# Kernel tuning notes

Hardware: AMD Instinct MI355X
Metric: run time of the kernel (lower is better)

Reference implementation:

```python
import jax, jax.numpy as jnp
import numpy as np

EPS = 1e-5

def conv1d(x, w, b, pad):
    # x: (B,Cin,T), w: (Cout,Cin,K)
    y = jax.lax.conv_general_dilated(x, w, (1,), [(pad, pad)],
                                     dimension_numbers=('NCW', 'OIW', 'NCW'))
    return y + b[None, :, None]

def group_norm(x, scale, bias, groups):
    B, C, T = x.shape
    xg = x.reshape(B, groups, C // groups, T)
    mu = xg.mean(axis=(2, 3), keepdims=True)
    var = xg.var(axis=(2, 3), keepdims=True)
    xn = ((xg - mu) * jax.lax.rsqrt(var + EPS)).reshape(B, C, T)
    return xn * scale[None, :, None] + bias[None, :, None]

def setup_inputs() -> dict:
    key = jax.random.key(0)
    ks = jax.random.split(key, 16)
    T, B = 1024, 128
    class_size, style_size, char_style_size = 80, 256, 64
    hidden, n_out = 128, 1
    cin = class_size + style_size + char_style_size  # 400
    def w(k, shape, fan_in):
        return jax.random.normal(k, shape, jnp.float32) * (1.0 / np.sqrt(fan_in))
    inp = {
        'input': jax.random.normal(ks[0], (T, B, class_size), jnp.float32),
        'g_style': jax.random.normal(ks[1], (B, style_size), jnp.float32),
        'spacing_style': jax.random.normal(ks[2], (B, 8), jnp.float32),
        'char_style': jax.random.normal(ks[3], (B, class_size, char_style_size), jnp.float32),
        'conv1_w': w(ks[4], (hidden, cin, 3), cin * 3),
        'conv1_b': jnp.zeros((hidden,), jnp.float32),
        'gn1_s': jnp.ones((hidden,), jnp.float32),
        'gn1_b': jnp.zeros((hidden,), jnp.float32),
        'conv2_w': w(ks[5], (hidden // 2, hidden, 3), hidden * 3),
        'conv2_b': jnp.zeros((hidden // 2,), jnp.float32),
        'gn2_s': jnp.ones((hidden // 2,), jnp.float32),
        'gn2_b': jnp.zeros((hidden // 2,), jnp.float32),
        'conv3_w': w(ks[6], (hidden // 4, hidden // 2, 3), (hidden // 2) * 3),
        'conv3_b': jnp.zeros((hidden // 4,), jnp.float32),
        'gn3_s': jnp.ones((hidden // 4,), jnp.float32),
        'gn3_b': jnp.zeros((hidden // 4,), jnp.float32),
        'conv4_w': w(ks[7], (n_out, hidden // 4, 1), hidden // 4),
        'conv4_b': jnp.zeros((n_out,), jnp.float32),
        'mean': jnp.full((1, n_out), 2.0, jnp.float32),
        'std': jnp.full((1, n_out), 1.0, jnp.float32),
    }
    return inp

def reference(input, g_style, spacing_style, char_style,
              conv1_w, conv1_b, gn1_s, gn1_b,
              conv2_w, conv2_b, gn2_s, gn2_b,
              conv3_w, conv3_b, gn3_s, gn3_b,
              conv4_w, conv4_b, mean, std):
    T, B, _ = input.shape
    # vectorized char-style gather (replaces the python double loop)
    text_chars = jnp.argmax(input, axis=2)                      # (T,B)
    input_style = char_style[jnp.arange(B)[None, :], text_chars]  # (T,B,Dc)
    gs = jnp.broadcast_to(g_style[None], (T,) + g_style.shape)    # (T,B,Ds)
    x = jnp.concatenate([input, gs, input_style], axis=2)         # (T,B,Cin)
    x = x.transpose(1, 2, 0)                                      # (B,Cin,T)
    x = jax.nn.relu(group_norm(conv1d(x, conv1_w, conv1_b, 1), gn1_s, gn1_b, 32))
    x = jax.nn.relu(group_norm(conv1d(x, conv2_w, conv2_b, 1), gn2_s, gn2_b, 32))
    x = jax.nn.relu(group_norm(conv1d(x, conv3_w, conv3_b, 1), gn3_s, gn3_b, 32))
    x = conv1d(x, conv4_w, conv4_b, 0)                            # (B,n_out,T)
    out = x.transpose(2, 0, 1)                                    # (T,B,n_out)
    return out * std + mean
```

## Files before the change

### kernel.cpp

```cpp
#include <hip/hip_runtime.h>
#include <hip/hip_bf16.h>

#define T_LEN 1024
#define BATCH 128
#define NM 131072

typedef __attribute__((ext_vector_type(8))) short short8;
typedef __attribute__((ext_vector_type(4))) float f32x4;

__device__ __forceinline__ float b2f(ushort u) {
  union { uint i; float f; } c; c.i = ((uint)u) << 16; return c.f;
}
__device__ __forceinline__ ushort f2b(float f) {
  __hip_bfloat16 h = __float2bfloat16(f);
  return *reinterpret_cast<ushort*>(&h);
}
__device__ __forceinline__ uint pack2(float a, float b) {
  return (uint)f2b(a) | ((uint)f2b(b) << 16);
}

__global__ __launch_bounds__(256) void k_prep(const float* __restrict__ gsty,
    const float* __restrict__ w1, const float* __restrict__ b1,
    const float* __restrict__ w2, const float* __restrict__ w3,
    float* __restrict__ Gfull, float* __restrict__ Gk0, float* __restrict__ Gk2,
    ushort* __restrict__ Wp1, ushort* __restrict__ Wp2, ushort* __restrict__ Wp3) {
  int bid = blockIdx.x, tid = threadIdx.x;
  if (bid < 128) {
    int b = bid;
    __shared__ float gl[256];
    gl[tid] = gsty[b*256 + tid];
    __syncthreads();
    if (tid < 128) {
      int o = tid;
      const float* wr = w1 + (size_t)o*1200 + 240;
      float s0 = 0.f, s1 = 0.f, s2 = 0.f;
      for (int c = 0; c < 256; ++c) {
        float g = gl[c];
        s0 += wr[c*3+0]*g; s1 += wr[c*3+1]*g; s2 += wr[c*3+2]*g;
      }
      Gk0[b*128+o] = s0;
      Gk2[b*128+o] = s2;
      Gfull[b*128+o] = s0 + s1 + s2 + b1[o];
    }
  } else {
    int e = (bid - 128)*256 + tid;
    if (e < 61440) {
      int o = e / 480, r = e % 480, k = r / 160, c = r % 160;
      float v = 0.f;
      if (c < 80)       v = w1[(size_t)o*1200 + c*3 + k];
      else if (c >= 96) v = w1[(size_t)o*1200 + (336 + (c-96))*3 + k];
      Wp1[e] = f2b(v);
    } else if (e < 61440 + 24576) {
      int e2 = e - 61440;
      int o = e2/384, r = e2%384, k = r/128, c = r%128;
      Wp2[e2] = f2b(w2[(size_t)o*384 + c*3 + k]);
    } else if (e < 61440 + 24576 + 6144) {
      int e3 = e - 61440 - 24576;
      int o = e3/192, r = e3%192, k = r/64, c = r%64;
      Wp3[e3] = f2b(w3[(size_t)o*192 + c*3 + k]);
    }
  }
}

__device__ __forceinline__ void c1_ldg(const float* __restrict__ inp, const float* __restrict__ cs,
                                       const int* idxs, int b, int cc, int t0, int task,
                                       float4& fa, float4& fb) {
  int r = task >> 2, q = task & 3;
  int t = t0 - 1 + r;
  fa = make_float4(0.f,0.f,0.f,0.f); fb = fa;
  if (t >= 0 && t < T_LEN) {
    const float* src;
    if (cc < 3) {
      int c8 = cc*32 + q*8;
      if (c8 >= 80) return;
      src = inp + ((size_t)t*BATCH + b)*80 + c8;
    } else {
      int jc = idxs[r];
      src = cs + ((size_t)b*80 + jc)*64 + (cc-3)*32 + q*8;
    }
    fa = *(const float4*)src;
    fb = *(const float4*)(src + 4);
  }
}
__device__ __forceinline__ void amax8(float& best, int& bi, float4 fa, float4 fb, int base, bool valid) {
  if (!valid) return;
  float v[8] = {fa.x, fa.y, fa.z, fa.w, fb.x, fb.y, fb.z, fb.w};
  #pragma unroll
  for (int i = 0; i < 8; ++i)
    if (v[i] > best) { best = v[i]; bi = base + i; }
}
__device__ __forceinline__ uint4 packf(float4 a, float4 b) {
  uint4 p;
  p.x = pack2(a.x, a.y); p.y = pack2(a.z, a.w);
  p.z = pack2(b.x, b.y); p.w = pack2(b.z, b.w);
  return p;
}
__device__ __forceinline__ short8 c1_ldw(const ushort* Wp1, int cc, int task) {
  int o = task / 12, seg = task % 12;
  int k = seg >> 2, oct = seg & 3;
  return *(const short8*)(Wp1 + (size_t)o*480 + k*160 + cc*32 + oct*8);
}
__device__ __forceinline__ void c1_wrx(ushort (*Xsb)[40], int task, uint4 v) {
  int r = task >> 2, q = task & 3;
  *(uint4*)&Xsb[r][q*8] = v;
}
__device__ __forceinline__ void c1_wrw(ushort (*Wsb)[104], int task, short8 v) {
  int o = task / 12, seg = task % 12;
  *(short8*)&Wsb[o][seg*8] = v;
}

__global__ __launch_bounds__(256) void k_conv1(const float* __restrict__ inp, const float* __restrict__ cs,
    const ushort* __restrict__ Wp1,
    const float* __restrict__ Gfull, const float* __restrict__ Gk0, const float* __restrict__ Gk2,
    ushort* __restrict__ y1, float2* __restrict__ part1) {
  __shared__ __align__(16) ushort Xs[2][130][40];
  __shared__ __align__(16) ushort Ws[2][128][104];
  __shared__ float gf[128], g0v[128], g2v[128];
  __shared__ float ps[4][128], pq[4][128];
  __shared__ int idxs[130];
  int b = blockIdx.x, tt = blockIdx.y;
  int t0 = tt * 128;
  int tid = threadIdx.x, lane = tid & 63, wave = tid >> 6;
  int ln = lane & 15, lq = lane >> 4, wt = wave * 32;
  int q = tid & 3, u = tid >> 2;

  if (tid < 128) {
    gf[tid]  = Gfull[b*128 + tid];
    g0v[tid] = Gk0[b*128 + tid];
    g2v[tid] = Gk2[b*128 + tid];
  }
  f32x4 acc[2][8];
  #pragma unroll
  for (int m = 0; m < 2; ++m)
    #pragma unroll
    for (int n = 0; n < 8; ++n) { f32x4 z = {0.f,0.f,0.f,0.f}; acc[m][n] = z; }

  float4 fa0, fb0, fa1, fb1, fa2, fb2;
  short8 rw[6];
  float bm0 = -1e30f, bm1 = -1e30f, bm2 = -1e30f;
  int ib0 = 0, ib1 = 0, ib2 = 0;

  c1_ldg(inp, cs, idxs, b, 0, t0, tid, fa0, fb0);
  c1_ldg(inp, cs, idxs, b, 0, t0, tid + 256, fa1, fb1);
  if (tid < 8) c1_ldg(inp, cs, idxs, b, 0, t0, tid + 512, fa2, fb2);
  amax8(bm0, ib0, fa0, fb0, q*8, true);
  amax8(bm1, ib1, fa1, fb1, q*8, true);
  if (tid < 8) amax8(bm2, ib2, fa2, fb2, q*8, true);
  #pragma unroll
  for (int i = 0; i < 6; ++i) rw[i] = c1_ldw(Wp1, 0, tid + i*256);
  c1_wrx(Xs[0], tid, packf(fa0, fb0));
  c1_wrx(Xs[0], tid + 256, packf(fa1, fb1));
  if (tid < 8) c1_wrx(Xs[0], tid + 512, packf(fa2, fb2));
  #pragma unroll
  for (int i = 0; i < 6; ++i) c1_wrw(Ws[0], tid + i*256, rw[i]);
  __syncthreads();

  for (int cc = 0; cc < 5; ++cc) {
    bool more = (cc < 4);
    if (more) {
      c1_ldg(inp, cs, idxs, b, cc+1, t0, tid, fa0, fb0);
      c1_ldg(inp, cs, idxs, b, cc+1, t0, tid + 256, fa1, fb1);
      if (tid < 8) c1_ldg(inp, cs, idxs, b, cc+1, t0, tid + 512, fa2, fb2);
      if (cc < 2) {
        int base = (cc+1)*32 + q*8;
        bool valid = (cc+1 < 2) || (q < 2);
        amax8(bm0, ib0, fa0, fb0, base, valid);
        amax8(bm1, ib1, fa1, fb1, base, valid);
        if (tid < 8) amax8(bm2, ib2, fa2, fb2, base, valid);
      }
      if (cc == 1) {
        #pragma unroll
        for (int d = 1; d <= 2; d <<= 1) {
          float ob; int oi;
          ob = __shfl_xor(bm0, d); oi = __shfl_xor(ib0, d);
          if (ob > bm0 || (ob == bm0 && oi < ib0)) { bm0 = ob; ib0 = oi; }
          ob = __shfl_xor(bm1, d); oi = __shfl_xor(ib1, d);
          if (ob > bm1 || (ob == bm1 && oi < ib1)) { bm1 = ob; ib1 = oi; }
          ob = __shfl_xor(bm2, d); oi = __shfl_xor(ib2, d);
          if (ob > bm2 || (ob == bm2 && oi < ib2)) { bm2 = ob; ib2 = oi; }
        }
        if (q == 0) { idxs[u] = ib0; idxs[u + 64] = ib1; }
        if (tid < 8 && (tid & 3) == 0) idxs[128 + (tid >> 2)] = ib2;
      }
      #pragma unroll
      for (int i = 0; i < 6; ++i) rw[i] = c1_ldw(Wp1, cc+1, tid + i*256);
    }
    int cur = cc & 1;
    #pragma unroll
    for (int k = 0; k < 3; ++k) {
      short8 a0 = *(const short8*)&Xs[cur][wt + ln + k][lq*8];
      short8 a1 = *(const short8*)&Xs[cur][wt + 16 + ln + k][lq*8];
      #pragma unroll
      for (int nt = 0; nt < 8; ++nt) {
        short8 bb = *(const short8*)&Ws[cur][nt*16 + ln][k*32 + lq*8];
        acc[0][nt] = __builtin_amdgcn_mfma_f32_16x16x32_bf16(a0, bb, acc[0][nt], 0, 0, 0);
        acc[1][nt] = __builtin_amdgcn_mfma_f32_16x16x32_bf16(a1, bb, acc[1][nt], 0, 0, 0);
      }
    }
    if (more) {
      int nxt = cur ^ 1;
      c1_wrx(Xs[nxt], tid, packf(fa0, fb0));
      c1_wrx(Xs[nxt], tid + 256, packf(fa1, fb1));
      if (tid < 8) c1_wrx(Xs[nxt], tid + 512, packf(fa2, fb2));
      #pragma unroll
      for (int i = 0; i < 6; ++i) c1_wrw(Ws[nxt], tid + i*256, rw[i]);
    }
    __syncthreads();
  }

  #pragma unroll
  for (int nt = 0; nt < 8; ++nt) {
    int o = nt*16 + ln;
    float add = gf[o];
    float s = 0.f, sq = 0.f;
    #pragma unroll
    for (int mt = 0; mt < 2; ++mt) {
      int tb = t0 + wt + mt*16 + lq*4;
      float vv[4];
      #pragma unroll
      for (int r = 0; r < 4; ++r) {
        float v = acc[mt][nt][r] + add;
        int t = tb + r;
        if (t == 0) v -= g0v[o];
        if (t == T_LEN-1) v -= g2v[o];
        vv[r] = v; s += v; sq += v*v;
      }
      uint2 pk;
      pk.x = pack2(vv[0], vv[1]);
      pk.y = pack2(vv[2], vv[3]);
      *(uint2*)(y1 + ((size_t)b*128 + o)*T_LEN + tb) = pk;
    }
    s  += __shfl_xor(s, 16);  s  += __shfl_xor(s, 32);
    sq += __shfl_xor(sq, 16); sq += __shfl_xor(sq, 32);
    if (lane < 16) { ps[wave][o] = s; pq[wave][o] = sq; }
  }
  __syncthreads();
  if (tid < 128) {
    float S = ps[0][tid]+ps[1][tid]+ps[2][tid]+ps[3][tid];
    float Q = pq[0][tid]+pq[1][tid]+pq[2][tid]+pq[3][tid];
    part1[((size_t)b*128 + tid)*8 + tt] = make_float2(S, Q);
  }
}

__device__ __forceinline__ short8 mid_ldw(const ushort* Wp, int cin, int cc, int task) {
  int o = task / 12, seg = task % 12;
  int k = seg >> 2, oct = seg & 3;
  return *(const short8*)(Wp + ((size_t)o*3 + k)*cin + cc*32 + oct*8);
}
__device__ __forceinline__ void mid_wrw(ushort (*Wsb)[104], int task, short8 v) {
  int o = task / 12, seg = task % 12;
  *(short8*)&Wsb[o][seg*8] = v;
}

template<int NC, int CO, int NT, int CPG>
__global__ __launch_bounds__(256) void k_convmid(const ushort* __restrict__ xin,
    const ushort* __restrict__ Wp, const float* __restrict__ bias,
    const float2* __restrict__ partin, const float* __restrict__ gs, const float* __restrict__ gb,
    ushort* __restrict__ yout, float2* __restrict__ part) {
  constexpr int CIN = NC*32;
  constexpr int NG = CIN/CPG;
  __shared__ __align__(16) ushort Xs[2][130][40];
  __shared__ __align__(16) ushort Ws[2][CO][104];
  __shared__ float2 affl[CIN];
  __shared__ float ssb[CIN], qqb[CIN];
  __shared__ float2 gmr[NG];
  __shared__ float bl[CO];
  __shared__ float ps[4][CO], pq[4][CO];
  int b = blockIdx.x, tt = blockIdx.y, t0 = tt*128;
  int tid = threadIdx.x, lane = tid & 63, wave = tid >> 6;
  int ln = lane & 15, lq = lane >> 4, wt = wave*32;
  int cp = (tid & 15)*2, j = tid >> 4;
  int er = (tid < 32) ? 0 : 129, eci = tid & 31;
  const ushort* xb = xin + (size_t)b * CIN * T_LEN;

  if (tid < CIN) {
    const float2* p = partin + (size_t)(b*CIN + tid)*8;
    float S = 0.f, Q = 0.f;
    #pragma unroll
    for (int j2 = 0; j2 < 8; ++j2) { float2 v = p[j2]; S += v.x; Q += v.y; }
    ssb[tid] = S; qqb[tid] = Q;
  }
  if (tid < CO)  bl[tid]  = bias[tid];

  f32x4 acc[2][NT];
  #pragma unroll
  for (int m = 0; m < 2; ++m)
    #pragma unroll
    for (int n = 0; n < NT; ++n) { f32x4 z = {0.f,0.f,0.f,0.f}; acc[m][n] = z; }

  short8 v0, v1;
  ushort ev = 0;
  short8 rw0, rw1, rw2;
  int te = t0 - 1 + er;

  {
    const ushort* s0 = xb + (size_t)cp * T_LEN + t0 + j*8;
    v0 = *(const short8*)s0;
    v1 = *(const short8*)(s0 + T_LEN);
    ev = 0;
    if (tid < 64 && te >= 0 && te < T_LEN) ev = xb[(size_t)eci * T_LEN + te];
    rw0 = mid_ldw(Wp, CIN, 0, tid);
    if constexpr (CO == 64) {
      rw1 = mid_ldw(Wp, CIN, 0, tid + 256);
      rw2 = mid_ldw(Wp, CIN, 0, tid + 512);
    } else {
      if (tid < 128) rw1 = mid_ldw(Wp, CIN, 0, tid + 256);
    }
  }
  __syncthreads();
  if (tid < NG) {
    float S = 0.f, Q = 0.f;
    #pragma unroll
    for (int ci = 0; ci < CPG; ++ci) { S += ssb[tid*CPG+ci]; Q += qqb[tid*CPG+ci]; }
    float invn = 1.f / (float)(CPG * T_LEN);
    float m = S * invn;
    float var = Q * invn - m*m;
    gmr[tid] = make_float2(m, rsqrtf(var + 1e-5f));
  }
  __syncthreads();
  if (tid < CIN) {
    float2 mr = gmr[tid / CPG];
    float a = mr.y * gs[tid];
    affl[tid] = make_float2(a, gb[tid] - mr.x * a);
  }
  __syncthreads();
  {
    float2 A0 = affl[cp], A1 = affl[cp+1];
    #pragma unroll
    for (int e = 0; e < 8; ++e) {
      float f0 = fmaxf(0.f, b2f((ushort)v0[e])*A0.x + A0.y);
      float f1 = fmaxf(0.f, b2f((ushort)v1[e])*A1.x + A1.y);
      *(uint*)&Xs[0][1 + j*8 + e][cp] = pack2(f0, f1);
    }
    if (tid < 64) {
      ushort val = 0;
      if (te >= 0 && te < T_LEN) { float2 A = affl[eci]; val = f2b(fmaxf(0.f, b2f(ev)*A.x + A.y)); }
      Xs[0][er][eci] = val;
    }
    mid_wrw(Ws[0], tid, rw0);
    if constexpr (CO == 64) {
      mid_wrw(Ws[0], tid + 256, rw1);
      mid_wrw(Ws[0], tid + 512, rw2);
    } else {
      if (tid < 128) mid_wrw(Ws[0], tid + 256, rw1);
    }
  }
  __syncthreads();

  for (int cc = 0; cc < NC; ++cc) {
    bool more = (cc + 1 < NC);
    if (more) {
      const ushort* s0 = xb + (size_t)((cc+1)*32 + cp) * T_LEN + t0 + j*8;
      v0 = *(const short8*)s0;
      v1 = *(const short8*)(s0 + T_LEN);
      ev = 0;
      if (tid < 64 && te >= 0 && te < T_LEN) ev = xb[(size_t)((cc+1)*32 + eci) * T_LEN + te];
      rw0 = mid_ldw(Wp, CIN, cc+1, tid);
      if constexpr (CO == 64) {
        rw1 = mid_ldw(Wp, CIN, cc+1, tid + 256);
        rw2 = mid_ldw(Wp, CIN, cc+1, tid + 512);
      } else {
        if (tid < 128) rw1 = mid_ldw(Wp, CIN, cc+1, tid + 256);
      }
    }
    int cur = cc & 1;
    #pragma unroll
    for (int k = 0; k < 3; ++k) {
      short8 a0 = *(const short8*)&Xs[cur][wt + ln + k][lq*8];
      short8 a1 = *(const short8*)&Xs[cur][wt + 16 + ln + k][lq*8];
      #pragma unroll
      for (int nt = 0; nt < NT; ++nt) {
        short8 bb = *(const short8*)&Ws[cur][nt*16 + ln][k*32 + lq*8];
        acc[0][nt] = __builtin_amdgcn_mfma_f32_16x16x32_bf16(a0, bb, acc[0][nt], 0, 0, 0);
        acc[1][nt] = __builtin_amdgcn_mfma_f32_16x16x32_bf16(a1, bb, acc[1][nt], 0, 0, 0);
      }
    }
    if (more) {
      int nxt = cur ^ 1;
      float2 A0 = affl[(cc+1)*32 + cp], A1 = affl[(cc+1)*32 + cp + 1];
      #pragma unroll
      for (int e = 0; e < 8; ++e) {
        float f0 = fmaxf(0.f, b2f((ushort)v0[e])*A0.x + A0.y);
        float f1 = fmaxf(0.f, b2f((ushort)v1[e])*A1.x + A1.y);
        *(uint*)&Xs[nxt][1 + j*8 + e][cp] = pack2(f0, f1);
      }
      if (tid < 64) {
        ushort val = 0;
        if (te >= 0 && te < T_LEN) { float2 A = affl[(cc+1)*32 + eci]; val = f2b(fmaxf(0.f, b2f(ev)*A.x + A.y)); }
        Xs[nxt][er][eci] = val;
      }
      mid_wrw(Ws[nxt], tid, rw0);
      if constexpr (CO == 64) {
        mid_wrw(Ws[nxt], tid + 256, rw1);
        mid_wrw(Ws[nxt], tid + 512, rw2);
      } else {
        if (tid < 128) mid_wrw(Ws[nxt], tid + 256, rw1);
      }
    }
    __syncthreads();
  }

  #pragma unroll
  for (int nt = 0; nt < NT; ++nt) {
    int o = nt*16 + ln;
    float add = bl[o];
    float s = 0.f, sq = 0.f;
    #pragma unroll
    for (int mt = 0; mt < 2; ++mt) {
      int tb = t0 + wt + mt*16 + lq*4;
      float vv[4];
      #pragma unroll
      for (int r = 0; r < 4; ++r) {
        float v = acc[mt][nt][r] + add;
        vv[r] = v; s += v; sq += v*v;
      }
      uint2 pk;
      pk.x = pack2(vv[0], vv[1]);
      pk.y = pack2(vv[2], vv[3]);
      *(uint2*)(yout + ((size_t)b*CO + o)*T_LEN + tb) = pk;
    }
    s  += __shfl_xor(s, 16);  s  += __shfl_xor(s, 32);
    sq += __shfl_xor(sq, 16); sq += __shfl_xor(sq, 32);
    if (lane < 16) { ps[wave][o] = s; pq[wave][o] = sq; }
  }
  __syncthreads();
  if (tid < CO) {
    float S = ps[0][tid]+ps[1][tid]+ps[2][tid]+ps[3][tid];
    float Q = pq[0][tid]+pq[1][tid]+pq[2][tid]+pq[3][tid];
    part[((size_t)b*CO + tid)*8 + tt] = make_float2(S, Q);
  }
}

__global__ __launch_bounds__(256) void k_final(const ushort* __restrict__ y3, const float2* __restrict__ part3,
    const float* __restrict__ s3, const float* __restrict__ b3,
    const float* __restrict__ w4, const float* __restrict__ b4,
    const float* __restrict__ mn, const float* __restrict__ sd, float* __restrict__ out) {
  int b = blockIdx.x;
  int t = blockIdx.y * 256 + threadIdx.x;
  __shared__ float wl[32];
  __shared__ float2 al[32];
  if (threadIdx.x < 32) {
    int c = threadIdx.x;
    const float2* p = part3 + (size_t)(b*32 + c)*8;
    float S = 0.f, Q = 0.f;
    #pragma unroll
    for (int j = 0; j < 8; ++j) { float2 v = p[j]; S += v.x; Q += v.y; }
    float invn = 1.f / (float)T_LEN;
    float m = S * invn;
    float var = Q * invn - m*m;
    float rs = rsqrtf(var + 1e-5f);
    float a = rs * s3[c];
    al[c] = make_float2(a, b3[c] - m*a);
    wl[c] = w4[c];
  }
  __syncthreads();
  float s = b4[0];
  #pragma unroll 8
  for (int c = 0; c < 32; ++c) {
    float v = b2f(y3[((size_t)b*32 + c)*T_LEN + t]);
    float2 A = al[c];
    s += wl[c] * fmaxf(0.f, v*A.x + A.y);
  }
  out[(size_t)t*BATCH + b] = s*sd[0] + mn[0];
}

extern "C" void kernel_launch(void* const* d_in, const int* in_sizes, int n_in,
                              void* d_out, int out_size, void* d_ws, size_t ws_size,
                              hipStream_t stream) {
  const float* inp  = (const float*)d_in[0];
  const float* gsty = (const float*)d_in[1];
  const float* cs   = (const float*)d_in[3];
  const float* w1   = (const float*)d_in[4];
  const float* b1   = (const float*)d_in[5];
  const float* gn1s = (const float*)d_in[6];
  const float* gn1b = (const float*)d_in[7];
  const float* w2   = (const float*)d_in[8];
  const float* b2   = (const float*)d_in[9];
  const float* gn2s = (const float*)d_in[10];
  const float* gn2b = (const float*)d_in[11];
  const float* w3   = (const float*)d_in[12];
  const float* b3   = (const float*)d_in[13];
  const float* gn3s = (const float*)d_in[14];
  const float* gn3b = (const float*)d_in[15];
  const float* w4   = (const float*)d_in[16];
  const float* b4   = (const float*)d_in[17];
  const float* mn   = (const float*)d_in[18];
  const float* sd   = (const float*)d_in[19];
  float* out = (float*)d_out;
  ushort* wsu = (ushort*)d_ws;

  ushort* Wp1 = wsu;
  ushort* Wp2 = Wp1 + 61440;
  ushort* Wp3 = Wp2 + 24576;
  float* Gfull = (float*)(Wp3 + 6144);
  float* Gk0   = Gfull + 16384;
  float* Gk2   = Gk0 + 16384;
  ushort* y1 = (ushort*)(Gk2 + 16384);
  ushort* y2 = y1 + (size_t)NM*128;
  ushort* y3 = y2 + (size_t)NM*64;
  float2* part1 = (float2*)(y3 + (size_t)NM*32);
  float2* part2 = part1 + 131072;
  float2* part3 = part2 + 65536;

  k_prep<<<488, 256, 0, stream>>>(gsty, w1, b1, w2, w3,
                                  Gfull, Gk0, Gk2, Wp1, Wp2, Wp3);
  k_conv1<<<dim3(128,8), 256, 0, stream>>>(inp, cs, Wp1, Gfull, Gk0, Gk2, y1, part1);
  k_convmid<4,64,4,4><<<dim3(128,8), 256, 0, stream>>>(y1, Wp2, b2, part1, gn1s, gn1b, y2, part2);
  k_convmid<2,32,2,2><<<dim3(128,8), 256, 0, stream>>>(y2, Wp3, b3, part2, gn2s, gn2b, y3, part3);
  k_final<<<dim3(128,4), 256, 0, stream>>>(y3, part3, gn3s, gn3b, w4, b4, mn, sd, out);
}
```

Baseline: 89.51 us.

## Store intermediate activations time-major via LDS-staged transposed epilogue

The bf16 intermediate activations between conv layers change from channel-major (B,C,T) to time-major (B,T,C). The epilogues stage outputs in shared memory (reusing the weight buffer) and write 16-byte coalesced rows. The mid-conv loader then reads contiguous 32-channel slices per time step, which replaces the strided per-channel loads and the separate halo scalar loads, and the final kernel reads each time row with four vector loads. The cost is an extra LDS round trip and barrier in the epilogue, and possible bank conflicts from the scattered 2-byte LDS stores.

```diff
diff --git a/kernel.cpp b/kernel.cpp
--- a/kernel.cpp
+++ b/kernel.cpp
@@ -208,6 +208,8 @@
     __syncthreads();
   }
 
+  ushort* Ts = &Ws[0][0][0];
+  constexpr int TP = 136;
   #pragma unroll
   for (int nt = 0; nt < 8; ++nt) {
     int o = nt*16 + ln;
@@ -215,26 +217,29 @@
     float s = 0.f, sq = 0.f;
     #pragma unroll
     for (int mt = 0; mt < 2; ++mt) {
-      int tb = t0 + wt + mt*16 + lq*4;
-      float vv[4];
+      int tl = wt + mt*16 + lq*4;
       #pragma unroll
       for (int r = 0; r < 4; ++r) {
         float v = acc[mt][nt][r] + add;
-        int t = tb + r;
+        int t = t0 + tl + r;
         if (t == 0) v -= g0v[o];
         if (t == T_LEN-1) v -= g2v[o];
-        vv[r] = v; s += v; sq += v*v;
-      }
-      uint2 pk;
-      pk.x = pack2(vv[0], vv[1]);
-      pk.y = pack2(vv[2], vv[3]);
-      *(uint2*)(y1 + ((size_t)b*128 + o)*T_LEN + tb) = pk;
+        s += v; sq += v*v;
+        Ts[(tl + r)*TP + o] = f2b(v);
+      }
     }
     s  += __shfl_xor(s, 16);  s  += __shfl_xor(s, 32);
     sq += __shfl_xor(sq, 16); sq += __shfl_xor(sq, 32);
     if (lane < 16) { ps[wave][o] = s; pq[wave][o] = sq; }
   }
   __syncthreads();
+  ushort* yb = y1 + ((size_t)b*1024 + t0)*128;
+  #pragma unroll
+  for (int it = 0; it < 8; ++it) {
+    int i = it*256 + tid;
+    int tl = i >> 4, c8 = (i & 15) * 8;
+    *(uint4*)(yb + tl*128 + c8) = *(const uint4*)(&Ts[tl*TP + c8]);
+  }
   if (tid < 128) {
     float S = ps[0][tid]+ps[1][tid]+ps[2][tid]+ps[3][tid];
     float Q = pq[0][tid]+pq[1][tid]+pq[2][tid]+pq[3][tid];
@@ -242,6 +247,32 @@
   }
 }
 
+__device__ __forceinline__ uint4 mid_ldx(const ushort* __restrict__ xb, int CINv, int cc, int t0, int task) {
+  int r = task >> 2, q = task & 3;
+  int t = t0 - 1 + r;
+  if (t >= 0 && t < T_LEN) return *(const uint4*)(xb + (size_t)t*CINv + cc*32 + q*8);
+  return make_uint4(0u,0u,0u,0u);
+}
+__device__ __forceinline__ void mid_wrx(ushort (*Xsb)[40], const float2* affl, int cbase,
+                                        int t0, int task, uint4 v) {
+  int r = task >> 2, q = task & 3;
+  int t = t0 - 1 + r;
+  uint4 w = make_uint4(0u,0u,0u,0u);
+  if (t >= 0 && t < T_LEN) {
+    const ushort* sv = (const ushort*)&v;
+    uint o[4];
+    #pragma unroll
+    for (int e = 0; e < 4; ++e) {
+      float2 A0 = affl[cbase + q*8 + 2*e];
+      float2 A1 = affl[cbase + q*8 + 2*e + 1];
+      float f0 = fmaxf(0.f, b2f(sv[2*e])*A0.x + A0.y);
+      float f1 = fmaxf(0.f, b2f(sv[2*e+1])*A1.x + A1.y);
+      o[e] = pack2(f0, f1);
+    }
+    w = make_uint4(o[0], o[1], o[2], o[3]);
+  }
+  *(uint4*)&Xsb[r][q*8] = w;
+}
 __device__ __forceinline__ short8 mid_ldw(const ushort* Wp, int cin, int cc, int task) {
   int o = task / 12, seg = task % 12;
   int k = seg >> 2, oct = seg & 3;
@@ -259,6 +290,7 @@
     ushort* __restrict__ yout, float2* __restrict__ part) {
   constexpr int CIN = NC*32;
   constexpr int NG = CIN/CPG;
+  constexpr int TP = CO + 8;
   __shared__ __align__(16) ushort Xs[2][130][40];
   __shared__ __align__(16) ushort Ws[2][CO][104];
   __shared__ float2 affl[CIN];
@@ -269,9 +301,7 @@
   int b = blockIdx.x, tt = blockIdx.y, t0 = tt*128;
   int tid = threadIdx.x, lane = tid & 63, wave = tid >> 6;
   int ln = lane & 15, lq = lane >> 4, wt = wave*32;
-  int cp = (tid & 15)*2, j = tid >> 4;
-  int er = (tid < 32) ? 0 : 129, eci = tid & 31;
-  const ushort* xb = xin + (size_t)b * CIN * T_LEN;
+  const ushort* xb = xin + (size_t)b * 1024 * CIN;
 
   if (tid < CIN) {
     const float2* p = partin + (size_t)(b*CIN + tid)*8;
@@ -288,24 +318,18 @@
     #pragma unroll
     for (int n = 0; n < NT; ++n) { f32x4 z = {0.f,0.f,0.f,0.f}; acc[m][n] = z; }
 
-  short8 v0, v1;
-  ushort ev = 0;
+  uint4 rx0, rx1, rx2;
   short8 rw0, rw1, rw2;
-  int te = t0 - 1 + er;
-
-  {
-    const ushort* s0 = xb + (size_t)cp * T_LEN + t0 + j*8;
-    v0 = *(const short8*)s0;
-    v1 = *(const short8*)(s0 + T_LEN);
-    ev = 0;
-    if (tid < 64 && te >= 0 && te < T_LEN) ev = xb[(size_t)eci * T_LEN + te];
-    rw0 = mid_ldw(Wp, CIN, 0, tid);
-    if constexpr (CO == 64) {
-      rw1 = mid_ldw(Wp, CIN, 0, tid + 256);
-      rw2 = mid_ldw(Wp, CIN, 0, tid + 512);
-    } else {
-      if (tid < 128) rw1 = mid_ldw(Wp, CIN, 0, tid + 256);
-    }
+
+  rx0 = mid_ldx(xb, CIN, 0, t0, tid);
+  rx1 = mid_ldx(xb, CIN, 0, t0, tid + 256);
+  if (tid < 8) rx2 = mid_ldx(xb, CIN, 0, t0, tid + 512);
+  rw0 = mid_ldw(Wp, CIN, 0, tid);
+  if constexpr (CO == 64) {
+    rw1 = mid_ldw(Wp, CIN, 0, tid + 256);
+    rw2 = mid_ldw(Wp, CIN, 0, tid + 512);
+  } else {
+    if (tid < 128) rw1 = mid_ldw(Wp, CIN, 0, tid + 256);
   }
   __syncthreads();
   if (tid < NG) {
@@ -324,37 +348,24 @@
     affl[tid] = make_float2(a, gb[tid] - mr.x * a);
   }
   __syncthreads();
-  {
-    float2 A0 = affl[cp], A1 = affl[cp+1];
-    #pragma unroll
-    for (int e = 0; e < 8; ++e) {
-      float f0 = fmaxf(0.f, b2f((ushort)v0[e])*A0.x + A0.y);
-      float f1 = fmaxf(0.f, b2f((ushort)v1[e])*A1.x + A1.y);
-      *(uint*)&Xs[0][1 + j*8 + e][cp] = pack2(f0, f1);
-    }
-    if (tid < 64) {
-      ushort val = 0;
-      if (te >= 0 && te < T_LEN) { float2 A = affl[eci]; val = f2b(fmaxf(0.f, b2f(ev)*A.x + A.y)); }
-      Xs[0][er][eci] = val;
-    }
-    mid_wrw(Ws[0], tid, rw0);
-    if constexpr (CO == 64) {
-      mid_wrw(Ws[0], tid + 256, rw1);
-      mid_wrw(Ws[0], tid + 512, rw2);
-    } else {
-      if (tid < 128) mid_wrw(Ws[0], tid + 256, rw1);
-    }
+  mid_wrx(Xs[0], affl, 0, t0, tid, rx0);
+  mid_wrx(Xs[0], affl, 0, t0, tid + 256, rx1);
+  if (tid < 8) mid_wrx(Xs[0], affl, 0, t0, tid + 512, rx2);
+  mid_wrw(Ws[0], tid, rw0);
+  if constexpr (CO == 64) {
+    mid_wrw(Ws[0], tid + 256, rw1);
+    mid_wrw(Ws[0], tid + 512, rw2);
+  } else {
+    if (tid < 128) mid_wrw(Ws[0], tid + 256, rw1);
   }
   __syncthreads();
 
   for (int cc = 0; cc < NC; ++cc) {
     bool more = (cc + 1 < NC);
     if (more) {
-      const ushort* s0 = xb + (size_t)((cc+1)*32 + cp) * T_LEN + t0 + j*8;
-      v0 = *(const short8*)s0;
-      v1 = *(const short8*)(s0 + T_LEN);
-      ev = 0;
-      if (tid < 64 && te >= 0 && te < T_LEN) ev = xb[(size_t)((cc+1)*32 + eci) * T_LEN + te];
+      rx0 = mid_ldx(xb, CIN, cc+1, t0, tid);
+      rx1 = mid_ldx(xb, CIN, cc+1, t0, tid + 256);
+      if (tid < 8) rx2 = mid_ldx(xb, CIN, cc+1, t0, tid + 512);
       rw0 = mid_ldw(Wp, CIN, cc+1, tid);
       if constexpr (CO == 64) {
         rw1 = mid_ldw(Wp, CIN, cc+1, tid + 256);
@@ -377,18 +388,9 @@
     }
     if (more) {
       int nxt = cur ^ 1;
-      float2 A0 = affl[(cc+1)*32 + cp], A1 = affl[(cc+1)*32 + cp + 1];
-      #pragma unroll
-      for (int e = 0; e < 8; ++e) {
-        float f0 = fmaxf(0.f, b2f((ushort)v0[e])*A0.x + A0.y);
-        float f1 = fmaxf(0.f, b2f((ushort)v1[e])*A1.x + A1.y);
-        *(uint*)&Xs[nxt][1 + j*8 + e][cp] = pack2(f0, f1);
-      }
-      if (tid < 64) {
-        ushort val = 0;
-        if (te >= 0 && te < T_LEN) { float2 A = affl[(cc+1)*32 + eci]; val = f2b(fmaxf(0.f, b2f(ev)*A.x + A.y)); }
-        Xs[nxt][er][eci] = val;
-      }
+      mid_wrx(Xs[nxt], affl, (cc+1)*32, t0, tid, rx0);
+      mid_wrx(Xs[nxt], affl, (cc+1)*32, t0, tid + 256, rx1);
+      if (tid < 8) mid_wrx(Xs[nxt], affl, (cc+1)*32, t0, tid + 512, rx2);
       mid_wrw(Ws[nxt], tid, rw0);
       if constexpr (CO == 64) {
         mid_wrw(Ws[nxt], tid + 256, rw1);
@@ -400,6 +402,7 @@
     __syncthreads();
   }
 
+  ushort* Ts = &Ws[0][0][0];
   #pragma unroll
   for (int nt = 0; nt < NT; ++nt) {
     int o = nt*16 + ln;
@@ -407,23 +410,27 @@
     float s = 0.f, sq = 0.f;
     #pragma unroll
     for (int mt = 0; mt < 2; ++mt) {
-      int tb = t0 + wt + mt*16 + lq*4;
-      float vv[4];
+      int tl = wt + mt*16 + lq*4;
       #pragma unroll
       for (int r = 0; r < 4; ++r) {
         float v = acc[mt][nt][r] + add;
-        vv[r] = v; s += v; sq += v*v;
-      }
-      uint2 pk;
-      pk.x = pack2(vv[0], vv[1]);
-      pk.y = pack2(vv[2], vv[3]);
-      *(uint2*)(yout + ((size_t)b*CO + o)*T_LEN + tb) = pk;
+        s += v; sq += v*v;
+        Ts[(tl + r)*TP + o] = f2b(v);
+      }
     }
     s  += __shfl_xor(s, 16);  s  += __shfl_xor(s, 32);
     sq += __shfl_xor(sq, 16); sq += __shfl_xor(sq, 32);
     if (lane < 16) { ps[wave][o] = s; pq[wave][o] = sq; }
   }
   __syncthreads();
+  ushort* yb = yout + ((size_t)b*1024 + t0)*CO;
+  constexpr int NCH = 128*CO/8;
+  #pragma unroll
+  for (int it = 0; it < NCH/256; ++it) {
+    int i = it*256 + tid;
+    int tl = i / (CO/8), c8 = (i % (CO/8)) * 8;
+    *(uint4*)(yb + tl*CO + c8) = *(const uint4*)(&Ts[tl*TP + c8]);
+  }
   if (tid < CO) {
     float S = ps[0][tid]+ps[1][tid]+ps[2][tid]+ps[3][tid];
     float Q = pq[0][tid]+pq[1][tid]+pq[2][tid]+pq[3][tid];
@@ -454,12 +461,19 @@
     wl[c] = w4[c];
   }
   __syncthreads();
+  const ushort* row = y3 + ((size_t)b*1024 + t)*32;
+  short8 v0 = *(const short8*)row;
+  short8 v1 = *(const short8*)(row + 8);
+  short8 v2 = *(const short8*)(row + 16);
+  short8 v3 = *(const short8*)(row + 24);
   float s = b4[0];
-  #pragma unroll 8
-  for (int c = 0; c < 32; ++c) {
-    float v = b2f(y3[((size_t)b*32 + c)*T_LEN + t]);
-    float2 A = al[c];
-    s += wl[c] * fmaxf(0.f, v*A.x + A.y);
+  #pragma unroll
+  for (int e = 0; e < 8; ++e) {
+    float2 A0 = al[e], A1 = al[8+e], A2 = al[16+e], A3 = al[24+e];
+    s += wl[e]    * fmaxf(0.f, b2f((ushort)v0[e])*A0.x + A0.y);
+    s += wl[8+e]  * fmaxf(0.f, b2f((ushort)v1[e])*A1.x + A1.y);
+    s += wl[16+e] * fmaxf(0.f, b2f((ushort)v2[e])*A2.x + A2.y);
+    s += wl[24+e] * fmaxf(0.f, b2f((ushort)v3[e])*A3.x + A3.y);
   }
   out[(size_t)t*BATCH + b] = s*sd[0] + mn[0];
 }
```

New measurement: 89.27 us. No clear change (-0.3%).
